# Kernel tuning notes

Measured on AMD Instinct MI355X. Metric: run time of the kernel, lower is better.

The kernel has to match this reference:

```python
import jax, jax.numpy as jnp
import numpy as np

N, E = 50000, 400000
EMB, IN, HID, HEADS = 128, 128, 128, 3
RRELU_SLOPE = (1.0 / 8.0 + 1.0 / 3.0) / 2.0  # torch.rrelu eval-mode slope


def _gat_conv(h_in, src, dst, W, a_src, a_dst, b, concat):
    """PyG-style GATConv. h_in: [N, F_in]; src/dst: [E'] (self-loops included)."""
    n = h_in.shape[0]
    h = (h_in @ W).reshape(n, HEADS, -1)            # [N, H, C]
    e_src = jnp.sum(h * a_src, axis=-1)             # [N, H]
    e_dst = jnp.sum(h * a_dst, axis=-1)             # [N, H]
    e = jax.nn.leaky_relu(e_src[src] + e_dst[dst], 0.2)  # [E', H]
    # softmax over incoming edges of each target node
    m = jax.ops.segment_max(e, dst, num_segments=n)
    ex = jnp.exp(e - m[dst])
    denom = jax.ops.segment_sum(ex, dst, num_segments=n)
    alpha = ex / denom[dst]                          # [E', H]
    out = jax.ops.segment_sum(h[src] * alpha[:, :, None], dst, num_segments=n)  # [N,H,C]
    out = out.reshape(n, -1) if concat else out.mean(axis=1)
    return out + b


def _rrelu(x):
    return jnp.where(x >= 0, x, x * RRELU_SLOPE)


def setup_inputs() -> dict:
    key = jax.random.key(0)
    ks = jax.random.split(key, 16)
    d_in = IN + EMB

    def glorot(k, shape):
        fan = sum(shape)
        return jax.random.normal(k, shape, jnp.float32) * np.sqrt(2.0 / fan)

    return {
        "z": jax.random.normal(ks[0], (N, EMB), jnp.float32),
        "x": jax.random.normal(ks[1], (N, IN), jnp.float32),
        "ei": jax.random.randint(ks[2], (2, E), 0, N, jnp.int32),
        "W1": glorot(ks[3], (d_in, HEADS * HID)),
        "a1_src": glorot(ks[4], (HEADS, HID)),
        "a1_dst": glorot(ks[5], (HEADS, HID)),
        "b1": jnp.zeros((HID,), jnp.float32),                 # concat=False -> size C
        "W2": glorot(ks[6], (HID, HEADS * HID)),
        "a2_src": glorot(ks[7], (HEADS, HID)),
        "a2_dst": glorot(ks[8], (HEADS, HID)),
        "b2": jnp.zeros((HEADS * HID,), jnp.float32),         # concat=True -> size H*C
        "W_lin": glorot(ks[9], (HEADS * HID, 1)),
        "b_lin": jnp.zeros((1,), jnp.float32),
    }


def reference(z, x, ei, W1, a1_src, a1_dst, b1, W2, a2_src, a2_dst, b2, W_lin, b_lin):
    n = x.shape[0]
    loops = jnp.arange(n, dtype=ei.dtype)
    src = jnp.concatenate([ei[0], loops])  # PyG add_self_loops=True
    dst = jnp.concatenate([ei[1], loops])
    h = jnp.concatenate([z, x], axis=1)
    h = _rrelu(_gat_conv(h, src, dst, W1, a1_src, a1_dst, b1, concat=False))
    h = _rrelu(_gat_conv(h, src, dst, W2, a2_src, a2_dst, b2, concat=True))
    return jax.nn.sigmoid(h @ W_lin + b_lin)
```

## Files before the change

kernel.cpp:

```cpp
#include <hip/hip_runtime.h>
#include <stdint.h>

#define HEADS 3
#define HID 128
#define FDIM (HEADS * HID)

typedef __attribute__((ext_vector_type(8))) short bf16x8;
typedef __attribute__((ext_vector_type(4))) float f32x4;

__device__ __forceinline__ float lrelu(float x) { return x >= 0.f ? x : 0.2f * x; }
__device__ __forceinline__ float rrelu(float x) {
    const float SLOPE = (1.0f / 8.0f + 1.0f / 3.0f) * 0.5f;
    return x >= 0.f ? x : SLOPE * x;
}
__device__ __forceinline__ unsigned short f2bf(float f) {
    union { float f; unsigned u; } c; c.f = f;
    unsigned r = c.u + 0x7FFF + ((c.u >> 16) & 1);
    return (unsigned short)(r >> 16);
}
__device__ __forceinline__ float bflo(unsigned u) {
    union { unsigned u; float f; } c; c.u = u << 16; return c.f;
}
__device__ __forceinline__ float bfhi(unsigned u) {
    union { unsigned u; float f; } c; c.u = u & 0xffff0000u; return c.f;
}

__device__ __forceinline__ void gload_lds16(const void* g, void* l) {
    __builtin_amdgcn_global_load_lds(
        (const __attribute__((address_space(1))) void*)g,
        (__attribute__((address_space(3))) void*)l, 16, 0, 0);
}


__global__ void k_hist(const int* __restrict__ dst, int E, int* __restrict__ cnt) {
    for (int i = blockIdx.x * blockDim.x + threadIdx.x; i < E; i += gridDim.x * blockDim.x)
        atomicAdd(&cnt[dst[i]], 1);
}

#define SC_T 256
#define SC_E 8
#define SC_CHUNK (SC_T * SC_E)

__global__ __launch_bounds__(SC_T) void k_scan1(const int* __restrict__ cnt,
                                                int* __restrict__ exc,
                                                int* __restrict__ bsum, int n) {
    __shared__ int sm[SC_T];
    int b = blockIdx.x, t = threadIdx.x;
    int base = b * SC_CHUNK + t * SC_E;
    int v[SC_E];
    int s = 0;
#pragma unroll
    for (int i = 0; i < SC_E; i++) {
        int idx = base + i;
        v[i] = (idx < n) ? cnt[idx] : 0;
        s += v[i];
    }
    sm[t] = s;
    __syncthreads();
    for (int off = 1; off < SC_T; off <<= 1) {
        int x = (t >= off) ? sm[t - off] : 0;
        __syncthreads();
        sm[t] += x;
        __syncthreads();
    }
    int run = sm[t] - s;
    if (t == SC_T - 1) bsum[b] = sm[t];
#pragma unroll
    for (int i = 0; i < SC_E; i++) {
        int idx = base + i;
        if (idx < n) exc[idx] = run;
        run += v[i];
    }
}

__global__ __launch_bounds__(256) void k_scan2(const int* __restrict__ bsum,
                                               int* __restrict__ bpre, int nb) {
    __shared__ int sm[256];
    int t = threadIdx.x;
    int v = (t < nb) ? bsum[t] : 0;
    sm[t] = v;
    __syncthreads();
    for (int off = 1; off < 256; off <<= 1) {
        int x = (t >= off) ? sm[t - off] : 0;
        __syncthreads();
        sm[t] += x;
        __syncthreads();
    }
    if (t < nb) bpre[t + 1] = sm[t];
    if (t == 0) bpre[0] = 0;
}

__global__ void k_scan3(int* __restrict__ offs, const int* __restrict__ bpre,
                        int* __restrict__ cursor, int n, int nb) {
    int i = blockIdx.x * blockDim.x + threadIdx.x;
    if (i < n) {
        int o = offs[i] + bpre[i / SC_CHUNK];
        offs[i] = o;
        cursor[i] = o;
    }
    if (i == 0) offs[n] = bpre[nb];
}

__global__ void k_scatter(const int* __restrict__ src, const int* __restrict__ dst, int E,
                          int* __restrict__ cursor, int* __restrict__ ssrc,
                          int* __restrict__ sdst) {
    for (int i = blockIdx.x * blockDim.x + threadIdx.x; i < E; i += gridDim.x * blockDim.x) {
        int d = dst[i];
        int p = atomicAdd(&cursor[d], 1);
        ssrc[p] = src[i];
        sdst[p] = d;
    }
}


__global__ void k_cvt_wt(const float* __restrict__ W, unsigned short* __restrict__ WT,
                         int K, int Ncols) {
    int n = blockIdx.x;
    for (int k = threadIdx.x; k < K; k += blockDim.x)
        WT[(size_t)n * K + k] = f2bf(W[(size_t)k * Ncols + n]);
}


template <bool F32A>
__global__ __launch_bounds__(256) void k_gemm(
    const void* __restrict__ Ap0, const void* __restrict__ Ap1, int Nn,
    const unsigned short* __restrict__ BT,
    unsigned short* __restrict__ C,
    int K, int Ncols,
    const float* __restrict__ asrc, const float* __restrict__ adst,
    float* __restrict__ es, float* __restrict__ ed, int Nnodes) {
    __shared__ __align__(16) unsigned short As[64 * 32];
    __shared__ __align__(16) unsigned short Bs[128 * 32];
    __shared__ float esP[64][2], edP[64][2];
    int tid = threadIdx.x;
    int w = tid >> 6, lane = tid & 63;
    int row0 = blockIdx.x * 64;
    int head = blockIdx.y;
    int col0 = head * 128;
    int wr = w >> 1, wc = w & 1;

    f32x4 acc[2][4] = {};
    int frow = lane & 15;
    int fk = (lane >> 4) * 8;

    const float* zf = (const float*)Ap0;
    const float* xf = (const float*)Ap1;
    float4 va[2];
    if (F32A) {
#pragma unroll
        for (int i = 0; i < 2; i++) {
            int idx = i * 256 + tid;
            int row = idx >> 3, c4 = (idx & 7) * 4;
            int gr = row0 + row;
            const float* sp = zf + (size_t)gr * 128 + c4;
            va[i] = (gr < Nn) ? *(const float4*)sp : make_float4(0.f, 0.f, 0.f, 0.f);
        }
    }

    for (int k0 = 0; k0 < K; k0 += 32) {
#pragma unroll
        for (int i = 0; i < 2; i++) {
            int c = (i * 4 + w) * 64 + lane;
            gload_lds16(BT + (size_t)(col0 + (c >> 2)) * K + k0 + (c & 3) * 8,
                        (char*)Bs + (i * 4 + w) * 1024);
        }
        if (F32A) {
#pragma unroll
            for (int i = 0; i < 2; i++) {
                int idx = i * 256 + tid;
                unsigned short o[4] = {f2bf(va[i].x), f2bf(va[i].y),
                                       f2bf(va[i].z), f2bf(va[i].w)};
                *(uint2*)((char*)As + (size_t)idx * 8) = *(uint2*)o;
            }
        } else {
            const unsigned short* A = (const unsigned short*)Ap0;
            int c = tid;
            gload_lds16(A + (size_t)(row0 + (c >> 2)) * K + k0 + (c & 3) * 8,
                        (char*)As + w * 1024);
        }
        asm volatile("s_waitcnt vmcnt(0)" ::: "memory");
        __syncthreads();

        if (F32A && (k0 + 32 < K)) {
            int kn = k0 + 32;
#pragma unroll
            for (int i = 0; i < 2; i++) {
                int idx = i * 256 + tid;
                int row = idx >> 3, c4 = (idx & 7) * 4;
                int gr = row0 + row;
                const float* sp = (kn < 128)
                                      ? (zf + (size_t)gr * 128 + kn + c4)
                                      : (xf + (size_t)gr * 128 + (kn - 128) + c4);
                va[i] = (gr < Nn) ? *(const float4*)sp : make_float4(0.f, 0.f, 0.f, 0.f);
            }
        }

        bf16x8 af[2], bfr[4];
#pragma unroll
        for (int m = 0; m < 2; m++)
            af[m] = *(const bf16x8*)&As[(wr * 32 + m * 16 + frow) * 32 + fk];
#pragma unroll
        for (int n = 0; n < 4; n++)
            bfr[n] = *(const bf16x8*)&Bs[(wc * 64 + n * 16 + frow) * 32 + fk];
#pragma unroll
        for (int m = 0; m < 2; m++)
#pragma unroll
            for (int n = 0; n < 4; n++)
                acc[m][n] = __builtin_amdgcn_mfma_f32_16x16x32_bf16(af[m], bfr[n], acc[m][n], 0, 0, 0);
        __syncthreads();
    }

    int ccol = lane & 15, crow = (lane >> 4) * 4;

#pragma unroll
    for (int m = 0; m < 2; m++)
#pragma unroll
        for (int n = 0; n < 4; n++)
#pragma unroll
            for (int j = 0; j < 4; j++) {
                int r = row0 + wr * 32 + m * 16 + crow + j;
                int cc = col0 + wc * 64 + n * 16 + ccol;
                C[(size_t)r * Ncols + cc] = f2bf(acc[m][n][j]);
            }

    float as4[4], ad4[4];
#pragma unroll
    for (int n = 0; n < 4; n++) {
        int col_sub = wc * 64 + n * 16 + ccol;
        as4[n] = asrc[head * HID + col_sub];
        ad4[n] = adst[head * HID + col_sub];
    }
#pragma unroll
    for (int m = 0; m < 2; m++)
#pragma unroll
        for (int j = 0; j < 4; j++) {
            float ps = 0.f, pd = 0.f;
#pragma unroll
            for (int n = 0; n < 4; n++) {
                float v = acc[m][n][j];
                ps = fmaf(v, as4[n], ps);
                pd = fmaf(v, ad4[n], pd);
            }
#pragma unroll
            for (int off = 1; off < 16; off <<= 1) {
                ps += __shfl_xor(ps, off);
                pd += __shfl_xor(pd, off);
            }
            if (ccol == 0) {
                int row_sub = wr * 32 + m * 16 + crow + j;
                esP[row_sub][wc] = ps;
                edP[row_sub][wc] = pd;
            }
        }
    __syncthreads();
    if (tid < 64) {
        int r = row0 + tid;
        if (r < Nnodes) {
            es[(size_t)r * 3 + head] = esP[tid][0] + esP[tid][1];
            ed[(size_t)r * 3 + head] = edP[tid][0] + edP[tid][1];
        }
    }
}


__global__ void k_edge_w(const int* __restrict__ ssrc, const int* __restrict__ sdst,
                         const float* __restrict__ es, const float* __restrict__ ed,
                         float4* __restrict__ w4, int E) {
    for (int j = blockIdx.x * blockDim.x + threadIdx.x; j < E; j += gridDim.x * blockDim.x) {
        int s = ssrc[j], d = sdst[j];
        float w0 = __expf(lrelu(es[s * 3 + 0] + ed[d * 3 + 0]));
        float w1 = __expf(lrelu(es[s * 3 + 1] + ed[d * 3 + 1]));
        float w2 = __expf(lrelu(es[s * 3 + 2] + ed[d * 3 + 2]));
        w4[j] = make_float4(w0, w1, w2, 0.f);
    }
}


#define EDGE_UNROLL4(body)                                                       \
    int j = j0;                                                                  \
    for (; j + 4 <= j1; j += 4) {                                                \
        int si[4]; float4 wv[4]; unsigned uu[4][3];                              \
        _Pragma("unroll") for (int e = 0; e < 4; e++) si[e] = ssrc[j + e];       \
        _Pragma("unroll") for (int e = 0; e < 4; e++) wv[e] = w4[j + e];         \
        _Pragma("unroll") for (int e = 0; e < 4; e++) {                          \
            const unsigned* rp = Hu + (size_t)si[e] * 192 + L;                   \
            uu[e][0] = rp[0]; uu[e][1] = rp[64]; uu[e][2] = rp[128];             \
        }                                                                        \
        _Pragma("unroll") for (int e = 0; e < 4; e++) { body(wv[e], uu[e]) }     \
    }                                                                            \
    for (; j < j1; j++) {                                                        \
        int s1_ = ssrc[j]; float4 w_ = w4[j];                                    \
        const unsigned* rp = Hu + (size_t)s1_ * 192 + L;                         \
        unsigned u_[3] = {rp[0], rp[64], rp[128]};                               \
        { body(w_, u_) }                                                         \
    }

#define ACC3(wv, uv)                                                             \
    a0[0] = fmaf(wv.x, bflo(uv[0]), a0[0]); a1[0] = fmaf(wv.x, bfhi(uv[0]), a1[0]); \
    a0[1] = fmaf(wv.y, bflo(uv[1]), a0[1]); a1[1] = fmaf(wv.y, bfhi(uv[1]), a1[1]); \
    a0[2] = fmaf(wv.z, bflo(uv[2]), a0[2]); a1[2] = fmaf(wv.z, bfhi(uv[2]), a1[2]); \
    den0 += wv.x; den1 += wv.y; den2 += wv.z;

__global__ __launch_bounds__(256) void k_agg_mean(const unsigned* __restrict__ Hu,
                                                  const float4* __restrict__ w4,
                                                  const float* __restrict__ es,
                                                  const float* __restrict__ ed,
                                                  const int* __restrict__ offs,
                                                  const int* __restrict__ ssrc,
                                                  const float* __restrict__ b,
                                                  unsigned* __restrict__ out, int Nn) {
    int L = threadIdx.x & 63;
    int wstep = gridDim.x * 4;
    for (int n = blockIdx.x * 4 + (threadIdx.x >> 6); n < Nn; n += wstep) {
        float s0 = __expf(lrelu(es[n * 3 + 0] + ed[n * 3 + 0]));
        float s1 = __expf(lrelu(es[n * 3 + 1] + ed[n * 3 + 1]));
        float s2 = __expf(lrelu(es[n * 3 + 2] + ed[n * 3 + 2]));
        float den0 = s0, den1 = s1, den2 = s2;
        const unsigned* rp = Hu + (size_t)n * 192 + L;
        unsigned u0 = rp[0], u1 = rp[64], u2 = rp[128];
        float a0[3] = {s0 * bflo(u0), s1 * bflo(u1), s2 * bflo(u2)};
        float a1[3] = {s0 * bfhi(u0), s1 * bfhi(u1), s2 * bfhi(u2)};
        int j0 = offs[n], j1 = offs[n + 1];
        EDGE_UNROLL4(ACC3)
        float iv0 = 1.f / den0, iv1 = 1.f / den1, iv2 = 1.f / den2;
        int c0 = 2 * L;
        float2 bb = *(const float2*)&b[c0];
        float m0 = (a0[0] * iv0 + a0[1] * iv1 + a0[2] * iv2) * (1.f / 3.f) + bb.x;
        float m1 = (a1[0] * iv0 + a1[1] * iv1 + a1[2] * iv2) * (1.f / 3.f) + bb.y;
        unsigned short o[2] = {f2bf(rrelu(m0)), f2bf(rrelu(m1))};
        out[(size_t)n * 64 + L] = *(unsigned*)o;
    }
}

__global__ __launch_bounds__(256) void k_agg_cat_final(const unsigned* __restrict__ Hu,
                                                       const float4* __restrict__ w4,
                                                       const float* __restrict__ es,
                                                       const float* __restrict__ ed,
                                                       const int* __restrict__ offs,
                                                       const int* __restrict__ ssrc,
                                                       const float* __restrict__ b,
                                                       const float* __restrict__ Wl,
                                                       const float* __restrict__ bl,
                                                       float* __restrict__ out, int Nn) {
    int L = threadIdx.x & 63;
    int wstep = gridDim.x * 4;
    for (int n = blockIdx.x * 4 + (threadIdx.x >> 6); n < Nn; n += wstep) {
        float s0 = __expf(lrelu(es[n * 3 + 0] + ed[n * 3 + 0]));
        float s1 = __expf(lrelu(es[n * 3 + 1] + ed[n * 3 + 1]));
        float s2 = __expf(lrelu(es[n * 3 + 2] + ed[n * 3 + 2]));
        float den0 = s0, den1 = s1, den2 = s2;
        const unsigned* rp = Hu + (size_t)n * 192 + L;
        unsigned u0 = rp[0], u1 = rp[64], u2 = rp[128];
        float a0[3] = {s0 * bflo(u0), s1 * bflo(u1), s2 * bflo(u2)};
        float a1[3] = {s0 * bfhi(u0), s1 * bfhi(u1), s2 * bfhi(u2)};
        int j0 = offs[n], j1 = offs[n + 1];
        EDGE_UNROLL4(ACC3)
        float ivv[3] = {1.f / den0, 1.f / den1, 1.f / den2};
        float p = 0.f;
#pragma unroll
        for (int k = 0; k < 3; k++) {
            int col = k * HID + 2 * L;
            float2 bb = *(const float2*)&b[col];
            float2 wl = *(const float2*)&Wl[col];
            float r0 = rrelu(a0[k] * ivv[k] + bb.x);
            float r1 = rrelu(a1[k] * ivv[k] + bb.y);
            p = fmaf(r0, wl.x, p);
            p = fmaf(r1, wl.y, p);
        }
#pragma unroll
        for (int off = 32; off > 0; off >>= 1) p += __shfl_down(p, off);
        if (L == 0) out[n] = 1.f / (1.f + __expf(-(p + bl[0])));
    }
}


extern "C" void kernel_launch(void* const* d_in, const int* in_sizes, int n_in,
                              void* d_out, int out_size, void* d_ws, size_t ws_size,
                              hipStream_t stream) {
    const float* z   = (const float*)d_in[0];
    const float* x   = (const float*)d_in[1];
    const int*   ei  = (const int*)d_in[2];
    const float* W1  = (const float*)d_in[3];
    const float* a1s = (const float*)d_in[4];
    const float* a1d = (const float*)d_in[5];
    const float* b1  = (const float*)d_in[6];
    const float* W2  = (const float*)d_in[7];
    const float* a2s = (const float*)d_in[8];
    const float* a2d = (const float*)d_in[9];
    const float* b2  = (const float*)d_in[10];
    const float* Wl  = (const float*)d_in[11];
    const float* bl  = (const float*)d_in[12];
    float* outp = (float*)d_out;

    int Nn = in_sizes[0] / 128;
    int E  = in_sizes[2] / 2;
    int Mpad = (Nn + 127) & ~127;
    int nb = (Nn + SC_CHUNK - 1) / SC_CHUNK;

    char* p = (char*)d_ws;
    auto carve = [&](size_t bytes) -> char* {
        char* r = p;
        p += (bytes + 255) & ~(size_t)255;
        return r;
    };
    int*            offs   = (int*)carve((size_t)(Nn + 1) * 4);
    int*            cursor = (int*)carve((size_t)Nn * 4);
    int*            ssrc   = (int*)carve((size_t)E * 4);
    int*            sdst   = (int*)carve((size_t)E * 4);
    int*            bsum   = (int*)carve((size_t)(nb + 1) * 4);
    int*            bpre   = (int*)carve((size_t)(nb + 1) * 4);
    float*          e1s    = (float*)carve((size_t)Nn * 3 * 4);
    float*          e1d    = (float*)carve((size_t)Nn * 3 * 4);
    float4*         w4     = (float4*)carve((size_t)E * 16);
    unsigned short* W1T    = (unsigned short*)carve((size_t)FDIM * 256 * 2);
    unsigned short* W2T    = (unsigned short*)carve((size_t)FDIM * 128 * 2);
    unsigned short* Hbf    = (unsigned short*)carve((size_t)Mpad * FDIM * 2);
    unsigned short* H2in   = (unsigned short*)carve((size_t)Mpad * 128 * 2);

    const int* srcI = ei;
    const int* dstI = ei + E;

    hipMemsetAsync(cursor, 0, (size_t)Nn * 4, stream);
    k_hist<<<1024, 256, 0, stream>>>(dstI, E, cursor);
    k_scan1<<<nb, SC_T, 0, stream>>>(cursor, offs, bsum, Nn);
    k_scan2<<<1, 256, 0, stream>>>(bsum, bpre, nb);
    k_scan3<<<(Nn + 255) / 256, 256, 0, stream>>>(offs, bpre, cursor, Nn, nb);
    k_scatter<<<1024, 256, 0, stream>>>(srcI, dstI, E, cursor, ssrc, sdst);

    k_cvt_wt<<<FDIM, 256, 0, stream>>>(W1, W1T, 256, FDIM);
    k_cvt_wt<<<FDIM, 128, 0, stream>>>(W2, W2T, 128, FDIM);
    hipMemsetAsync(H2in + (size_t)Nn * 128, 0, (size_t)(Mpad - Nn) * 128 * 2, stream);

    dim3 gg(Mpad / 64, FDIM / 128);

    k_gemm<true><<<gg, 256, 0, stream>>>(z, x, Nn, W1T, Hbf, 256, FDIM,
                                         a1s, a1d, e1s, e1d, Nn);
    k_edge_w<<<1024, 256, 0, stream>>>(ssrc, sdst, e1s, e1d, w4, E);
    k_agg_mean<<<2048, 256, 0, stream>>>((const unsigned*)Hbf, w4, e1s, e1d, offs,
                                         ssrc, b1, (unsigned*)H2in, Nn);

    k_gemm<false><<<gg, 256, 0, stream>>>(H2in, nullptr, Mpad, W2T, Hbf, 128, FDIM,
                                          a2s, a2d, e1s, e1d, Nn);
    k_edge_w<<<1024, 256, 0, stream>>>(ssrc, sdst, e1s, e1d, w4, E);
    k_agg_cat_final<<<2048, 256, 0, stream>>>((const unsigned*)Hbf, w4, e1s, e1d, offs,
                                              ssrc, b2, Wl, bl, outp, Nn);
}
```

Measured before the change: 248.5 us.

## Fuse edge-weight computation into aggregation kernels and pad attention scores to float4

Removes the separate k_edge_w kernels and the per-edge float4 weight buffer. Edge softmax weights are now recomputed inside the aggregation loops from per-node attention scores, which are stored with a stride of 4 so they load as a single float4. The sorted-destination array is dropped from the scatter. This trades two kernel launches and the E×16-byte weight writes and reads for redundant exp work across the 64 lanes of each wave and an extra gathered float4 load per edge.

```diff
diff --git a/kernel.cpp b/kernel.cpp
--- a/kernel.cpp
+++ b/kernel.cpp
@@ -102,13 +102,11 @@
 }
 
 __global__ void k_scatter(const int* __restrict__ src, const int* __restrict__ dst, int E,
-                          int* __restrict__ cursor, int* __restrict__ ssrc,
-                          int* __restrict__ sdst) {
+                          int* __restrict__ cursor, int* __restrict__ ssrc) {
     for (int i = blockIdx.x * blockDim.x + threadIdx.x; i < E; i += gridDim.x * blockDim.x) {
         int d = dst[i];
         int p = atomicAdd(&cursor[d], 1);
         ssrc[p] = src[i];
-        sdst[p] = d;
     }
 }
 
@@ -256,53 +254,49 @@
     if (tid < 64) {
         int r = row0 + tid;
         if (r < Nnodes) {
-            es[(size_t)r * 3 + head] = esP[tid][0] + esP[tid][1];
-            ed[(size_t)r * 3 + head] = edP[tid][0] + edP[tid][1];
-        }
-    }
-}
-
-
-__global__ void k_edge_w(const int* __restrict__ ssrc, const int* __restrict__ sdst,
-                         const float* __restrict__ es, const float* __restrict__ ed,
-                         float4* __restrict__ w4, int E) {
-    for (int j = blockIdx.x * blockDim.x + threadIdx.x; j < E; j += gridDim.x * blockDim.x) {
-        int s = ssrc[j], d = sdst[j];
-        float w0 = __expf(lrelu(es[s * 3 + 0] + ed[d * 3 + 0]));
-        float w1 = __expf(lrelu(es[s * 3 + 1] + ed[d * 3 + 1]));
-        float w2 = __expf(lrelu(es[s * 3 + 2] + ed[d * 3 + 2]));
-        w4[j] = make_float4(w0, w1, w2, 0.f);
-    }
-}
-
-
-#define EDGE_UNROLL4(body)                                                       \
+            es[(size_t)r * 4 + head] = esP[tid][0] + esP[tid][1];
+            ed[(size_t)r * 4 + head] = edP[tid][0] + edP[tid][1];
+        }
+    }
+}
+
+
+#define EDGE_LOOP(body)                                                          \
     int j = j0;                                                                  \
     for (; j + 4 <= j1; j += 4) {                                                \
-        int si[4]; float4 wv[4]; unsigned uu[4][3];                              \
+        int si[4]; float4 ef[4]; unsigned uu[4][3];                              \
         _Pragma("unroll") for (int e = 0; e < 4; e++) si[e] = ssrc[j + e];       \
-        _Pragma("unroll") for (int e = 0; e < 4; e++) wv[e] = w4[j + e];         \
         _Pragma("unroll") for (int e = 0; e < 4; e++) {                          \
             const unsigned* rp = Hu + (size_t)si[e] * 192 + L;                   \
             uu[e][0] = rp[0]; uu[e][1] = rp[64]; uu[e][2] = rp[128];             \
         }                                                                        \
-        _Pragma("unroll") for (int e = 0; e < 4; e++) { body(wv[e], uu[e]) }     \
+        _Pragma("unroll") for (int e = 0; e < 4; e++)                            \
+            ef[e] = *(const float4*)&es[(size_t)si[e] * 4];                      \
+        _Pragma("unroll") for (int e = 0; e < 4; e++) {                          \
+            float w0 = __expf(lrelu(ef[e].x + edn.x));                           \
+            float w1 = __expf(lrelu(ef[e].y + edn.y));                           \
+            float w2 = __expf(lrelu(ef[e].z + edn.z));                           \
+            body(w0, w1, w2, uu[e])                                              \
+        }                                                                        \
     }                                                                            \
     for (; j < j1; j++) {                                                        \
-        int s1_ = ssrc[j]; float4 w_ = w4[j];                                    \
-        const unsigned* rp = Hu + (size_t)s1_ * 192 + L;                         \
+        int s_ = ssrc[j];                                                        \
+        const unsigned* rp = Hu + (size_t)s_ * 192 + L;                          \
         unsigned u_[3] = {rp[0], rp[64], rp[128]};                               \
-        { body(w_, u_) }                                                         \
-    }
-
-#define ACC3(wv, uv)                                                             \
-    a0[0] = fmaf(wv.x, bflo(uv[0]), a0[0]); a1[0] = fmaf(wv.x, bfhi(uv[0]), a1[0]); \
-    a0[1] = fmaf(wv.y, bflo(uv[1]), a0[1]); a1[1] = fmaf(wv.y, bfhi(uv[1]), a1[1]); \
-    a0[2] = fmaf(wv.z, bflo(uv[2]), a0[2]); a1[2] = fmaf(wv.z, bfhi(uv[2]), a1[2]); \
-    den0 += wv.x; den1 += wv.y; den2 += wv.z;
+        float4 ef_ = *(const float4*)&es[(size_t)s_ * 4];                        \
+        float w0 = __expf(lrelu(ef_.x + edn.x));                                 \
+        float w1 = __expf(lrelu(ef_.y + edn.y));                                 \
+        float w2 = __expf(lrelu(ef_.z + edn.z));                                 \
+        { body(w0, w1, w2, u_) }                                                 \
+    }
+
+#define ACC3(w0, w1, w2, uv)                                                     \
+    a0[0] = fmaf(w0, bflo(uv[0]), a0[0]); a1[0] = fmaf(w0, bfhi(uv[0]), a1[0]);  \
+    a0[1] = fmaf(w1, bflo(uv[1]), a0[1]); a1[1] = fmaf(w1, bfhi(uv[1]), a1[1]);  \
+    a0[2] = fmaf(w2, bflo(uv[2]), a0[2]); a1[2] = fmaf(w2, bfhi(uv[2]), a1[2]);  \
+    den0 += w0; den1 += w1; den2 += w2;
 
 __global__ __launch_bounds__(256) void k_agg_mean(const unsigned* __restrict__ Hu,
-                                                  const float4* __restrict__ w4,
                                                   const float* __restrict__ es,
                                                   const float* __restrict__ ed,
                                                   const int* __restrict__ offs,
@@ -312,16 +306,18 @@
     int L = threadIdx.x & 63;
     int wstep = gridDim.x * 4;
     for (int n = blockIdx.x * 4 + (threadIdx.x >> 6); n < Nn; n += wstep) {
-        float s0 = __expf(lrelu(es[n * 3 + 0] + ed[n * 3 + 0]));
-        float s1 = __expf(lrelu(es[n * 3 + 1] + ed[n * 3 + 1]));
-        float s2 = __expf(lrelu(es[n * 3 + 2] + ed[n * 3 + 2]));
+        float4 edn = *(const float4*)&ed[(size_t)n * 4];
+        float4 esn = *(const float4*)&es[(size_t)n * 4];
+        float s0 = __expf(lrelu(esn.x + edn.x));
+        float s1 = __expf(lrelu(esn.y + edn.y));
+        float s2 = __expf(lrelu(esn.z + edn.z));
         float den0 = s0, den1 = s1, den2 = s2;
         const unsigned* rp = Hu + (size_t)n * 192 + L;
         unsigned u0 = rp[0], u1 = rp[64], u2 = rp[128];
         float a0[3] = {s0 * bflo(u0), s1 * bflo(u1), s2 * bflo(u2)};
         float a1[3] = {s0 * bfhi(u0), s1 * bfhi(u1), s2 * bfhi(u2)};
         int j0 = offs[n], j1 = offs[n + 1];
-        EDGE_UNROLL4(ACC3)
+        EDGE_LOOP(ACC3)
         float iv0 = 1.f / den0, iv1 = 1.f / den1, iv2 = 1.f / den2;
         int c0 = 2 * L;
         float2 bb = *(const float2*)&b[c0];
@@ -333,7 +329,6 @@
 }
 
 __global__ __launch_bounds__(256) void k_agg_cat_final(const unsigned* __restrict__ Hu,
-                                                       const float4* __restrict__ w4,
                                                        const float* __restrict__ es,
                                                        const float* __restrict__ ed,
                                                        const int* __restrict__ offs,
@@ -345,16 +340,18 @@
     int L = threadIdx.x & 63;
     int wstep = gridDim.x * 4;
     for (int n = blockIdx.x * 4 + (threadIdx.x >> 6); n < Nn; n += wstep) {
-        float s0 = __expf(lrelu(es[n * 3 + 0] + ed[n * 3 + 0]));
-        float s1 = __expf(lrelu(es[n * 3 + 1] + ed[n * 3 + 1]));
-        float s2 = __expf(lrelu(es[n * 3 + 2] + ed[n * 3 + 2]));
+        float4 edn = *(const float4*)&ed[(size_t)n * 4];
+        float4 esn = *(const float4*)&es[(size_t)n * 4];
+        float s0 = __expf(lrelu(esn.x + edn.x));
+        float s1 = __expf(lrelu(esn.y + edn.y));
+        float s2 = __expf(lrelu(esn.z + edn.z));
         float den0 = s0, den1 = s1, den2 = s2;
         const unsigned* rp = Hu + (size_t)n * 192 + L;
         unsigned u0 = rp[0], u1 = rp[64], u2 = rp[128];
         float a0[3] = {s0 * bflo(u0), s1 * bflo(u1), s2 * bflo(u2)};
         float a1[3] = {s0 * bfhi(u0), s1 * bfhi(u1), s2 * bfhi(u2)};
         int j0 = offs[n], j1 = offs[n + 1];
-        EDGE_UNROLL4(ACC3)
+        EDGE_LOOP(ACC3)
         float ivv[3] = {1.f / den0, 1.f / den1, 1.f / den2};
         float p = 0.f;
 #pragma unroll
@@ -406,12 +403,10 @@
     int*            offs   = (int*)carve((size_t)(Nn + 1) * 4);
     int*            cursor = (int*)carve((size_t)Nn * 4);
     int*            ssrc   = (int*)carve((size_t)E * 4);
-    int*            sdst   = (int*)carve((size_t)E * 4);
     int*            bsum   = (int*)carve((size_t)(nb + 1) * 4);
     int*            bpre   = (int*)carve((size_t)(nb + 1) * 4);
-    float*          e1s    = (float*)carve((size_t)Nn * 3 * 4);
-    float*          e1d    = (float*)carve((size_t)Nn * 3 * 4);
-    float4*         w4     = (float4*)carve((size_t)E * 16);
+    float*          e1s    = (float*)carve((size_t)Mpad * 16);
+    float*          e1d    = (float*)carve((size_t)Mpad * 16);
     unsigned short* W1T    = (unsigned short*)carve((size_t)FDIM * 256 * 2);
     unsigned short* W2T    = (unsigned short*)carve((size_t)FDIM * 128 * 2);
     unsigned short* Hbf    = (unsigned short*)carve((size_t)Mpad * FDIM * 2);
@@ -425,7 +420,7 @@
     k_scan1<<<nb, SC_T, 0, stream>>>(cursor, offs, bsum, Nn);
     k_scan2<<<1, 256, 0, stream>>>(bsum, bpre, nb);
     k_scan3<<<(Nn + 255) / 256, 256, 0, stream>>>(offs, bpre, cursor, Nn, nb);
-    k_scatter<<<1024, 256, 0, stream>>>(srcI, dstI, E, cursor, ssrc, sdst);
+    k_scatter<<<1024, 256, 0, stream>>>(srcI, dstI, E, cursor, ssrc);
 
     k_cvt_wt<<<FDIM, 256, 0, stream>>>(W1, W1T, 256, FDIM);
     k_cvt_wt<<<FDIM, 128, 0, stream>>>(W2, W2T, 128, FDIM);
@@ -435,13 +430,11 @@
 
     k_gemm<true><<<gg, 256, 0, stream>>>(z, x, Nn, W1T, Hbf, 256, FDIM,
                                          a1s, a1d, e1s, e1d, Nn);
-    k_edge_w<<<1024, 256, 0, stream>>>(ssrc, sdst, e1s, e1d, w4, E);
-    k_agg_mean<<<2048, 256, 0, stream>>>((const unsigned*)Hbf, w4, e1s, e1d, offs,
+    k_agg_mean<<<2048, 256, 0, stream>>>((const unsigned*)Hbf, e1s, e1d, offs,
                                          ssrc, b1, (unsigned*)H2in, Nn);
 
     k_gemm<false><<<gg, 256, 0, stream>>>(H2in, nullptr, Mpad, W2T, Hbf, 128, FDIM,
                                           a2s, a2d, e1s, e1d, Nn);
-    k_edge_w<<<1024, 256, 0, stream>>>(ssrc, sdst, e1s, e1d, w4, E);
-    k_agg_cat_final<<<2048, 256, 0, stream>>>((const unsigned*)Hbf, w4, e1s, e1d, offs,
+    k_agg_cat_final<<<2048, 256, 0, stream>>>((const unsigned*)Hbf, e1s, e1d, offs,
                                               ssrc, b2, Wl, bl, outp, Nn);
 }
```

Result: no change. 253.1 us (+1.9%).
